# Performance work log

Measured on AMD Instinct MI355X. Metric: run time of the kernel, lower is better.

## Reference

```python
import jax, jax.numpy as jnp
import numpy as np

B, IN, ED, PW, OUT, CL, NK = 2048, 4096, 8192, 2048, 256, 16, 32
MIX = 0.5

def _onehot_mask(key, n):
    # near-one-hot selector matrix [n, NK], as built by forward_update_masks
    idx = jax.random.choice(key, n, (NK,), replace=False)
    return jnp.zeros((n, NK), jnp.float32).at[idx, jnp.arange(NK)].set(1.0)

def setup_inputs():
    ks = jax.random.split(jax.random.key(0), 24)
    f = jnp.float32
    adj = (jax.random.uniform(ks[4], (IN, IN)) < 0.01).astype(f)
    adj = jnp.maximum(adj, adj.T).at[jnp.arange(IN), jnp.arange(IN)].set(1.0)
    return {
        'x_gene': jax.random.normal(ks[0], (B, IN), f),
        'x_invmea': jax.random.normal(ks[1], (B, IN), f),
        'x_curv': jax.random.normal(ks[2], (B, ED), f),
        'clinn': jax.random.normal(ks[3], (B, CL), f),
        'Adj': adj,
        'edge_mask': (jax.random.uniform(ks[5], (ED, IN)) < 0.005).astype(f),
        'pathway_mask': (jax.random.uniform(ks[6], (PW, ED)) < 0.02).astype(f),
        'top_gene_mask': _onehot_mask(ks[7], IN),
        'top_invmea_mask': _onehot_mask(ks[8], IN),
        'top_curv_mask': _onehot_mask(ks[9], ED),
        'top_path_mask': _onehot_mask(ks[10], PW),
        'W1': jnp.full((IN, IN), 0.05, f),
        'b1': 0.01 * jax.random.normal(ks[11], (IN,), f),
        'W2': jnp.full((ED, IN), 0.05, f),
        'b2': 0.01 * jax.random.normal(ks[12], (ED,), f),
        'W3': jnp.full((PW, ED), 0.05, f),
        'b3': 0.01 * jax.random.normal(ks[13], (PW,), f),
        'W4': 0.02 * jax.random.normal(ks[14], (OUT, PW), f),
        'b4': 0.01 * jax.random.normal(ks[15], (OUT,), f),
        'W5': 0.02 * jax.random.normal(ks[16], (OUT, OUT), f),
        'b5': 0.01 * jax.random.normal(ks[17], (OUT,), f),
        'W6': 0.05 * jax.random.normal(ks[18], (OUT, OUT + CL + 4 * NK), f),
        'W7': 0.05 * jax.random.normal(ks[19], (1, OUT), f),
        'mp11': MIX * jnp.ones(IN, f),
        'mp12': (1.0 - MIX) * jnp.ones(IN, f),
        'mp1': jnp.ones(IN, f),
        'mp21': MIX * jnp.ones(ED, f),
        'mp22': (1.0 - MIX) * jnp.ones(ED, f),
        'mp2': jnp.ones(ED, f),
        'mp3': jnp.ones(PW, f),
    }

def reference(x_gene, x_invmea, x_curv, clinn, Adj, edge_mask, pathway_mask,
              top_gene_mask, top_invmea_mask, top_curv_mask, top_path_mask,
              W1, b1, W2, b2, W3, b3, W4, b4, W5, b5, W6, W7,
              mp11, mp12, mp1, mp21, mp22, mp2, mp3):
    sg = jax.lax.stop_gradient
    sig = jax.nn.sigmoid
    kept_gene = sg(x_gene @ top_gene_mask)                     # [B,NK] gather-as-matmul
    x1 = sig(x_gene @ (W1 * Adj).T + b1)                       # masked linear [B,IN]
    x1 = x_invmea * (mp11 * mp1) + x1 * (mp12 * mp1)
    kept_invmea = sg(x1 @ top_invmea_mask)
    x1 = sig(x1 @ (W2 * edge_mask).T + b2)                     # [B,ED]
    x1 = x_curv * (mp21 * mp2) + x1 * (mp22 * mp2)
    kept_curv = sg(x1 @ top_curv_mask)
    x1 = sig(x1 @ (W3 * pathway_mask).T + b3)                  # [B,PW]
    x1 = x1 * mp3
    kept_path = sg(x1 @ top_path_mask)
    x1 = sig(x1 @ W4.T + b4)
    x1 = sig(x1 @ W5.T + b5)                                   # [B,OUT]
    x_cat = jnp.concatenate([x1, kept_gene, kept_invmea, kept_curv, kept_path, clinn], axis=1)
    lp = sig(x_cat @ W6.T)
    lp = lp - jnp.mean(lp, axis=1, keepdims=True)
    return lp @ W7.T                                           # [B,1]
```

## Files before the change

kernel.cpp:

```cpp
#include <hip/hip_runtime.h>

typedef unsigned short u16;
typedef __attribute__((ext_vector_type(4))) float f32x4;
typedef __attribute__((ext_vector_type(8))) short s16x8;

__device__ __forceinline__ u16 f2bf(float f) {
    union { float f; unsigned u; } c; c.f = f;
    return (u16)((c.u + 0x7fffu + ((c.u >> 16) & 1u)) >> 16);
}
__device__ __forceinline__ float bf2f(u16 u) {
    union { unsigned u; float f; } c; c.u = ((unsigned)u) << 16; return c.f;
}
__device__ __forceinline__ unsigned pk2(float a, float b) {
    return (unsigned)f2bf(a) | ((unsigned)f2bf(b) << 16);
}
__device__ __forceinline__ float sigm(float x) { return 1.0f / (1.0f + __expf(-x)); }

__device__ __forceinline__ void load16_g2l(const void* g, void* l) {
    __builtin_amdgcn_global_load_lds(
        (const __attribute__((address_space(1))) unsigned int*)(unsigned long long)g,
        (__attribute__((address_space(3))) unsigned int*)(unsigned int)(unsigned long long)l,
        16, 0, 0);
}

__global__ __launch_bounds__(256) void convF(const float* __restrict__ in,
                                             u16* __restrict__ out, unsigned n8) {
    unsigned i = blockIdx.x * 256u + threadIdx.x;
    if (i >= n8) return;
    float4 a = ((const float4*)in)[2 * i];
    float4 b = ((const float4*)in)[2 * i + 1];
    uint4 o;
    o.x = pk2(a.x, a.y); o.y = pk2(a.z, a.w);
    o.z = pk2(b.x, b.y); o.w = pk2(b.z, b.w);
    ((uint4*)out)[i] = o;
}

__global__ __launch_bounds__(256) void transpF(const float* __restrict__ in,
                                               u16* __restrict__ out, int Rr, int Cc) {
    __shared__ float t[64][65];
    const int r0 = blockIdx.y * 64, c0 = blockIdx.x * 64;
    const int tid = threadIdx.x;
#pragma unroll
    for (int i = 0; i < 16; i++) {
        int idx = tid + i * 256;
        int rr = idx >> 6, cc = idx & 63;
        t[rr][cc] = in[(size_t)(r0 + rr) * Cc + c0 + cc];
    }
    __syncthreads();
#pragma unroll
    for (int i = 0; i < 16; i++) {
        int idx = tid + i * 256;
        int cc = idx >> 6, rr = idx & 63;
        out[(size_t)(c0 + cc) * Rr + r0 + rr] = f2bf(t[rr][cc]);
    }
}

__global__ __launch_bounds__(256) void transpB(const u16* __restrict__ in,
                                               u16* __restrict__ out, int Rr, int Cc) {
    __shared__ u16 t[64][66];
    const int r0 = blockIdx.y * 64, c0 = blockIdx.x * 64;
    const int tid = threadIdx.x;
#pragma unroll
    for (int i = 0; i < 16; i++) {
        int idx = tid + i * 256;
        int rr = idx >> 6, cc = idx & 63;
        t[rr][cc] = in[(size_t)(r0 + rr) * Cc + c0 + cc];
    }
    __syncthreads();
#pragma unroll
    for (int i = 0; i < 16; i++) {
        int idx = tid + i * 256;
        int cc = idx >> 6, rr = idx & 63;
        out[(size_t)(c0 + cc) * Rr + r0 + rr] = t[rr][cc];
    }
}

__global__ __launch_bounds__(256) void ell_build(const float* __restrict__ M,
                                                 const float* __restrict__ W,
                                                 unsigned* __restrict__ ell,
                                                 int* __restrict__ cnt,
                                                 int C, int PAD, int R) {
    const int lane = threadIdx.x & 63;
    const int row = blockIdx.x * 4 + (threadIdx.x >> 6);
    if (row >= R) return;
    const float* mrow = M + (size_t)row * C;
    const float* wrow = W + (size_t)row * C;
    int n = 0;
    for (int c = lane * 4; c < C; c += 256) {
        float4 m = *(const float4*)(mrow + c);
        n += (m.x != 0.f) + (m.y != 0.f) + (m.z != 0.f) + (m.w != 0.f);
    }
    int pre = n;
#pragma unroll
    for (int off = 1; off < 64; off <<= 1) {
        int t = __shfl_up(pre, off, 64);
        if (lane >= off) pre += t;
    }
    int s = pre - n;
    unsigned* erow = ell + (size_t)row * PAD;
    for (int c = lane * 4; c < C; c += 256) {
        float4 m = *(const float4*)(mrow + c);
        if (m.x != 0.f) { if (s < PAD) erow[s] = ((unsigned)f2bf(wrow[c + 0]) << 16) | (unsigned)(c + 0); s++; }
        if (m.y != 0.f) { if (s < PAD) erow[s] = ((unsigned)f2bf(wrow[c + 1]) << 16) | (unsigned)(c + 1); s++; }
        if (m.z != 0.f) { if (s < PAD) erow[s] = ((unsigned)f2bf(wrow[c + 2]) << 16) | (unsigned)(c + 2); s++; }
        if (m.w != 0.f) { if (s < PAD) erow[s] = ((unsigned)f2bf(wrow[c + 3]) << 16) | (unsigned)(c + 3); s++; }
    }
    int tot = __shfl(pre, 63, 64);
    if (lane == 0) cnt[row] = tot > PAD ? PAD : tot;
}

template <int BPL>
__global__ __launch_bounds__(256) void spmm(const unsigned* __restrict__ ell,
                                            const int* __restrict__ cnt,
                                            const u16* __restrict__ xT,
                                            u16* __restrict__ outT,
                                            const float* __restrict__ bias,
                                            const float* __restrict__ c1a,
                                            const float* __restrict__ c1b,
                                            const float* __restrict__ c2a,
                                            const float* __restrict__ c2b,
                                            const u16* __restrict__ invT,
                                            int PAD) {
    const int lane = threadIdx.x & 63;
    const int wv = __builtin_amdgcn_readfirstlane((int)(threadIdx.x >> 6));
    const int j = blockIdx.y * 4 + wv;
    const int b0 = blockIdx.x * (64 * BPL) + lane * BPL;

    const unsigned* ep = ell + (size_t)j * PAD;
    int len = cnt[j];
    if (len > PAD) len = PAD;

    float acc[BPL];
#pragma unroll
    for (int i = 0; i < BPL; i++) acc[i] = 0.f;

    auto body = [&](unsigned e) {
        const int k = (int)(e & 0xFFFFu);
        union { float f; unsigned u; } w; w.u = (e >> 16) << 16;
        const u16* xp = xT + (size_t)k * 2048 + b0;
        if (BPL == 4) {
            uint2 xv = *(const uint2*)xp;
            union { float f; unsigned u; } f0, f1, f2, f3;
            f0.u = xv.x << 16; f1.u = xv.x & 0xFFFF0000u;
            f2.u = xv.y << 16; f3.u = xv.y & 0xFFFF0000u;
            acc[0] += w.f * f0.f; acc[1] += w.f * f1.f;
            acc[2] += w.f * f2.f; acc[3] += w.f * f3.f;
        } else {
            unsigned xv = *(const unsigned*)xp;
            union { float f; unsigned u; } f0, f1;
            f0.u = xv << 16; f1.u = xv & 0xFFFF0000u;
            acc[0] += w.f * f0.f; acc[1] += w.f * f1.f;
        }
    };
    int s = 0;
    for (; s + 4 <= len; s += 4) {
        unsigned e0 = ep[s], e1 = ep[s + 1], e2 = ep[s + 2], e3 = ep[s + 3];
        body(e0); body(e1); body(e2); body(e3);
    }
    for (; s < len; ++s) body(ep[s]);

    const float bi = bias[j];
    float c1 = 0.f;
    if (c1a) { c1 = c1a[j]; if (c1b) c1 *= c1b[j]; }
    float c2 = 1.f;
    if (c2a) { c2 = c2a[j]; if (c2b) c2 *= c2b[j]; }

    float v[BPL];
#pragma unroll
    for (int i = 0; i < BPL; i++) v[i] = sigm(acc[i] + bi) * c2;
    if (invT) {
        const u16* ip = invT + (size_t)j * 2048 + b0;
        if (BPL == 4) {
            uint2 iv = *(const uint2*)ip;
            union { float f; unsigned u; } g0, g1, g2, g3;
            g0.u = iv.x << 16; g1.u = iv.x & 0xFFFF0000u;
            g2.u = iv.y << 16; g3.u = iv.y & 0xFFFF0000u;
            v[0] += g0.f * c1; v[1] += g1.f * c1;
            v[2] += g2.f * c1; v[3] += g3.f * c1;
        } else {
            unsigned iv = *(const unsigned*)ip;
            union { float f; unsigned u; } g0, g1;
            g0.u = iv << 16; g1.u = iv & 0xFFFF0000u;
            v[0] += g0.f * c1; v[1] += g1.f * c1;
        }
    }
    u16* op = outT + (size_t)j * 2048 + b0;
    if (BPL == 4) {
        uint2 ov; ov.x = pk2(v[0], v[1]); ov.y = pk2(v[2], v[3]);
        *(uint2*)op = ov;
    } else {
        *(unsigned*)op = pk2(v[0], v[1]);
    }
}

__global__ void init_idx(int* __restrict__ idx) {
    if (threadIdx.x < 128) idx[threadIdx.x] = 0;
}

__global__ __launch_bounds__(256) void find_idx(const float* __restrict__ mask,
                                                int n, int* __restrict__ out) {
    int k = blockIdx.x;
    for (int i = threadIdx.x; i < n; i += 256)
        if (mask[(size_t)i * 32 + k] != 0.0f) out[k] = i;
}

__global__ __launch_bounds__(256) void gatherFT(const float* __restrict__ src, int ld,
                                                const int* __restrict__ idx,
                                                u16* __restrict__ dstT) {
    int i = blockIdx.x * 256 + threadIdx.x;
    int kk = i >> 11, b = i & 2047;
    dstT[i] = f2bf(src[(size_t)b * ld + idx[kk]]);
}
__global__ __launch_bounds__(256) void gatherT(const u16* __restrict__ xT,
                                               const int* __restrict__ idx,
                                               u16* __restrict__ dstT) {
    int i = blockIdx.x * 256 + threadIdx.x;
    int kk = i >> 11, b = i & 2047;
    dstT[i] = xT[(size_t)idx[kk] * 2048 + b];
}

__global__ __launch_bounds__(256) void build_xcat(float* __restrict__ xcat,
                                                  const u16* __restrict__ x5,
                                                  const u16* __restrict__ kgT,
                                                  const u16* __restrict__ kiT,
                                                  const u16* __restrict__ kcT,
                                                  const u16* __restrict__ kpT,
                                                  const float* __restrict__ clinn) {
    int i = blockIdx.x * 256 + threadIdx.x;
    if (i >= 2048 * 400) return;
    int b = i / 400, c = i - b * 400;
    float v;
    if (c < 256)      v = bf2f(x5[b * 256 + c]);
    else if (c < 288) v = bf2f(kgT[(c - 256) * 2048 + b]);
    else if (c < 320) v = bf2f(kiT[(c - 288) * 2048 + b]);
    else if (c < 352) v = bf2f(kcT[(c - 320) * 2048 + b]);
    else if (c < 384) v = bf2f(kpT[(c - 352) * 2048 + b]);
    else              v = clinn[b * 16 + (c - 384)];
    xcat[i] = v;
}

template <int WR, int WC, int MF, int NF, int KC, int WPE>
__global__ __launch_bounds__(WR * WC * 64, WPE)
void gemm_t(const u16* __restrict__ A, const u16* __restrict__ W,
            u16* __restrict__ Out, const float* __restrict__ bias, int N, int K) {
    constexpr int NTHR = WR * WC * 64;
    constexpr int BM = WR * MF * 16;
    constexpr int BN = WC * NF * 16;
    constexpr int BK = KC * 32;
    constexpr int CPR = KC * 4;
    constexpr int MSK = CPR - 1;
    constexpr int CA = BM * CPR / NTHR;
    constexpr int CB = BN * CPR / NTHR;
    constexpr int L  = CA + CB;

    __shared__ u16 At[2][BM * BK];
    __shared__ u16 Bt[2][BN * BK];

    const int tid = threadIdx.x;
    const int lane = tid & 63;
    const int wave = tid >> 6;
    const int wr = wave / WC, wc = wave % WC;
    const int tn = blockIdx.x, tm = blockIdx.y;
    const int r16 = lane & 15;
    const int q = lane >> 4;

    const u16* aSrc[CA]; int aDst[CA];
#pragma unroll
    for (int j = 0; j < CA; j++) {
        int c = tid + j * NTHR;
        int r = c / CPR, p = c - r * CPR;
        aSrc[j] = A + (size_t)(tm * BM + r) * K + (p ^ (r & MSK)) * 8;
        aDst[j] = c * 8;
    }
    const u16* bSrc[CB]; int bDst[CB];
#pragma unroll
    for (int j = 0; j < CB; j++) {
        int c = tid + j * NTHR;
        int r = c / CPR, p = c - r * CPR;
        bSrc[j] = W + (size_t)(tn * BN + r) * K + (p ^ (r & MSK)) * 8;
        bDst[j] = c * 8;
    }
    int aRd[MF][KC], bRd[NF][KC];
#pragma unroll
    for (int mi = 0; mi < MF; mi++)
#pragma unroll
        for (int kc = 0; kc < KC; kc++)
            aRd[mi][kc] = (wr * MF * 16 + mi * 16 + r16) * BK + (((kc * 4 + q) ^ (r16 & MSK)) << 3);
#pragma unroll
    for (int ni = 0; ni < NF; ni++)
#pragma unroll
        for (int kc = 0; kc < KC; kc++)
            bRd[ni][kc] = (wc * NF * 16 + ni * 16 + r16) * BK + (((kc * 4 + q) ^ (r16 & MSK)) << 3);

    const int nIter = K / BK;

#define ISSUE(slot, it_)                                              \
    do {                                                              \
        const int k0_ = (it_) * BK;                                   \
        _Pragma("unroll")                                             \
        for (int j = 0; j < CA; j++)                                  \
            load16_g2l(aSrc[j] + k0_, &At[slot][aDst[j]]);            \
        _Pragma("unroll")                                             \
        for (int j = 0; j < CB; j++)                                  \
            load16_g2l(bSrc[j] + k0_, &Bt[slot][bDst[j]]);            \
    } while (0)

    ISSUE(0, 0);
    if (nIter > 1) ISSUE(1, 1);

    f32x4 acc[MF][NF];
#pragma unroll
    for (int i = 0; i < MF; i++)
#pragma unroll
        for (int j = 0; j < NF; j++) acc[i][j] = (f32x4){0.f, 0.f, 0.f, 0.f};

    for (int it = 0; it < nIter; ++it) {
        const int s = it & 1;
        if (it + 1 < nIter) __builtin_amdgcn_s_waitcnt(0xF70 | L);
        else                __builtin_amdgcn_s_waitcnt(0xF70);
        __asm__ volatile("" ::: "memory");
        __builtin_amdgcn_s_barrier();
        __asm__ volatile("" ::: "memory");

        s16x8 af[KC][MF], bfr[KC][NF];
#pragma unroll
        for (int kc = 0; kc < KC; kc++) {
#pragma unroll
            for (int mi = 0; mi < MF; mi++) af[kc][mi] = *(const s16x8*)(&At[s][aRd[mi][kc]]);
#pragma unroll
            for (int ni = 0; ni < NF; ni++) bfr[kc][ni] = *(const s16x8*)(&Bt[s][bRd[ni][kc]]);
        }
        __asm__ volatile("" ::: "memory");
        __builtin_amdgcn_s_waitcnt(0xC07F);
        __builtin_amdgcn_s_barrier();
        __asm__ volatile("" ::: "memory");

        if (it + 2 < nIter) ISSUE(s, it + 2);

#pragma unroll
        for (int kc = 0; kc < KC; kc++)
#pragma unroll
            for (int mi = 0; mi < MF; mi++)
#pragma unroll
                for (int ni = 0; ni < NF; ni++)
                    acc[mi][ni] = __builtin_amdgcn_mfma_f32_16x16x32_bf16(af[kc][mi], bfr[kc][ni], acc[mi][ni], 0, 0, 0);
    }
#undef ISSUE

#pragma unroll
    for (int ni = 0; ni < NF; ni++) {
        const int n = tn * BN + wc * NF * 16 + ni * 16 + r16;
        const float bi = bias ? bias[n] : 0.f;
#pragma unroll
        for (int mi = 0; mi < MF; mi++) {
#pragma unroll
            for (int rg = 0; rg < 4; rg++) {
                const int m = tm * BM + wr * MF * 16 + mi * 16 + q * 4 + rg;
                Out[(size_t)m * N + n] = f2bf(sigm(acc[mi][ni][rg] + bi));
            }
        }
    }
}

__global__ __launch_bounds__(256) void tail_k(const float* __restrict__ xcat,
                                              const float* __restrict__ W6,
                                              const float* __restrict__ W7,
                                              float* __restrict__ out) {
    __shared__ float xs[8 * 400];
    __shared__ float s1[4][8], s2[4][8], s3[4];
    const int tid = threadIdx.x;
    const int b0 = blockIdx.x * 8;
    for (int i = tid; i < 8 * 400; i += 256) {
        int r = i / 400, k = i - r * 400;
        xs[i] = xcat[(size_t)(b0 + r) * 400 + k];
    }
    __syncthreads();
    const int j = tid;
    float acc[8];
#pragma unroll
    for (int r = 0; r < 8; r++) acc[r] = 0.f;
    const float4* wrow = (const float4*)(W6 + (size_t)j * 400);
    for (int c = 0; c < 100; c++) {
        float4 wv = wrow[c];
        const float* wp = (const float*)&wv;
#pragma unroll
        for (int t = 0; t < 4; t++) {
            float w = wp[t];
            int k = c * 4 + t;
#pragma unroll
            for (int r = 0; r < 8; r++) acc[r] += w * xs[r * 400 + k];
        }
    }
    const float w7j = W7[j];
    const int lane = tid & 63, wave = tid >> 6;
    float t3 = w7j;
#pragma unroll
    for (int off = 32; off > 0; off >>= 1) t3 += __shfl_down(t3, off, 64);
    if (lane == 0) s3[wave] = t3;
#pragma unroll
    for (int r = 0; r < 8; r++) {
        float lp = sigm(acc[r]);
        float t1 = lp, t2 = lp * w7j;
#pragma unroll
        for (int off = 32; off > 0; off >>= 1) {
            t1 += __shfl_down(t1, off, 64);
            t2 += __shfl_down(t2, off, 64);
        }
        if (lane == 0) { s1[wave][r] = t1; s2[wave][r] = t2; }
    }
    __syncthreads();
    if (tid < 8) {
        float S1 = s1[0][tid] + s1[1][tid] + s1[2][tid] + s1[3][tid];
        float S2 = s2[0][tid] + s2[1][tid] + s2[2][tid] + s2[3][tid];
        float SW = s3[0] + s3[1] + s3[2] + s3[3];
        out[b0 + tid] = S2 - (S1 * (1.f / 256.f)) * SW;
    }
}

extern "C" void kernel_launch(void* const* d_in, const int* in_sizes, int n_in,
                              void* d_out, int out_size, void* d_ws, size_t ws_size,
                              hipStream_t stream) {
    const float* x_gene   = (const float*)d_in[0];
    const float* x_invmea = (const float*)d_in[1];
    const float* x_curv   = (const float*)d_in[2];
    const float* clinn    = (const float*)d_in[3];
    const float* Adj      = (const float*)d_in[4];
    const float* edge_m   = (const float*)d_in[5];
    const float* path_m   = (const float*)d_in[6];
    const float* tg_mask  = (const float*)d_in[7];
    const float* ti_mask  = (const float*)d_in[8];
    const float* tc_mask  = (const float*)d_in[9];
    const float* tp_mask  = (const float*)d_in[10];
    const float* W1 = (const float*)d_in[11];  const float* b1 = (const float*)d_in[12];
    const float* W2 = (const float*)d_in[13];  const float* b2 = (const float*)d_in[14];
    const float* W3 = (const float*)d_in[15];  const float* b3 = (const float*)d_in[16];
    const float* W4 = (const float*)d_in[17];  const float* b4 = (const float*)d_in[18];
    const float* W5 = (const float*)d_in[19];  const float* b5 = (const float*)d_in[20];
    const float* W6 = (const float*)d_in[21];
    const float* W7 = (const float*)d_in[22];
    const float* mp11 = (const float*)d_in[23];
    const float* mp12 = (const float*)d_in[24];
    const float* mp1  = (const float*)d_in[25];
    const float* mp21 = (const float*)d_in[26];
    const float* mp22 = (const float*)d_in[27];
    const float* mp2  = (const float*)d_in[28];
    const float* mp3  = (const float*)d_in[29];

    char* ws = (char*)d_ws;
    const float* nulf = nullptr;
    float* out = (float*)d_out;

    u16*  xTg   = (u16*)(ws + 0);
    float* xcat = (float*)(ws + 0);
    u16*  xinvT = (u16*)(ws + 16777216);
    u16*  xcvT  = (u16*)(ws + 33554432);
    u16*  x1T   = (u16*)(ws + 67108864);
    u16*  x2T   = (u16*)(ws + 83886080);
    u16*  x3T   = (u16*)(ws + 117440512);
    u16*  x3    = (u16*)(ws + 125829120);
    unsigned* ell1 = (unsigned*)(ws + 134217728);
    unsigned* ell2 = (unsigned*)(ws + 138412032);
    unsigned* ell3 = (unsigned*)(ws + 141557760);
    int* cnt1 = (int*)(ws + 144179200);
    int* cnt2 = (int*)(ws + 144195584);
    int* cnt3 = (int*)(ws + 144228352);
    int* idxg = (int*)(ws + 144236544);
    int* idxi = idxg + 32;
    int* idxc = idxg + 64;
    int* idxp = idxg + 96;
    u16* kgT  = (u16*)(ws + 144237056);
    u16* kiT  = (u16*)(ws + 144368128);
    u16* kcT  = (u16*)(ws + 144499200);
    u16* kpT  = (u16*)(ws + 144630272);
    u16* w4b  = (u16*)(ws + 144761344);
    u16* w5b  = (u16*)(ws + 145809920);
    u16* x4   = (u16*)(ws + 145940992);
    u16* x5   = (u16*)(ws + 146989568);

    init_idx<<<1, 128, 0, stream>>>(idxg);
    find_idx<<<32, 256, 0, stream>>>(tg_mask, 4096, idxg);
    find_idx<<<32, 256, 0, stream>>>(ti_mask, 4096, idxi);
    find_idx<<<32, 256, 0, stream>>>(tc_mask, 8192, idxc);
    find_idx<<<32, 256, 0, stream>>>(tp_mask, 2048, idxp);
    gatherFT<<<256, 256, 0, stream>>>(x_gene, 4096, idxg, kgT);

    transpF<<<dim3(64, 32), 256, 0, stream>>>(x_gene, xTg, 2048, 4096);
    transpF<<<dim3(64, 32), 256, 0, stream>>>(x_invmea, xinvT, 2048, 4096);
    transpF<<<dim3(128, 32), 256, 0, stream>>>(x_curv, xcvT, 2048, 8192);

    ell_build<<<1024, 256, 0, stream>>>(Adj,    W1, ell1, cnt1, 4096, 256, 4096);
    ell_build<<<2048, 256, 0, stream>>>(edge_m, W2, ell2, cnt2, 4096,  96, 8192);
    ell_build<<<512,  256, 0, stream>>>(path_m, W3, ell3, cnt3, 8192, 320, 2048);

    convF<<<256, 256, 0, stream>>>(W4, w4b, 65536u);
    convF<<<32, 256, 0, stream>>>(W5, w5b, 8192u);

    spmm<4><<<dim3(8, 1024), 256, 0, stream>>>(ell1, cnt1, xTg, x1T, b1,
                                               mp11, mp1, mp12, mp1, xinvT, 256);
    gatherT<<<256, 256, 0, stream>>>(x1T, idxi, kiT);

    spmm<4><<<dim3(8, 2048), 256, 0, stream>>>(ell2, cnt2, x1T, x2T, b2,
                                               mp21, mp2, mp22, mp2, xcvT, 96);
    gatherT<<<256, 256, 0, stream>>>(x2T, idxc, kcT);

    spmm<2><<<dim3(16, 512), 256, 0, stream>>>(ell3, cnt3, x2T, x3T, b3,
                                               nulf, nulf, mp3, nulf, (const u16*)nullptr, 320);
    gatherT<<<256, 256, 0, stream>>>(x3T, idxp, kpT);
    transpB<<<dim3(32, 32), 256, 0, stream>>>(x3T, x3, 2048, 2048);

    gemm_t<2, 4, 4, 2, 2, 4><<<dim3(2, 16), 512, 0, stream>>>(x3, w4b, x4, b4, 256, 2048);
    gemm_t<2, 4, 4, 2, 2, 4><<<dim3(2, 16), 512, 0, stream>>>(x4, w5b, x5, b5, 256, 256);

    build_xcat<<<3200, 256, 0, stream>>>(xcat, x5, kgT, kiT, kcT, kpT, clinn);
    tail_k<<<256, 256, 0, stream>>>(xcat, W6, W7, out);
}
```

Measured before the change: 1.016 ms.

## Merge index-finding kernels, use nontemporal spmm I/O, shrink gemm tiles

Replaces the init plus four find_idx launches with a single find_all kernel that does a block-wide max reduction. The spmm epilogue now uses nontemporal loads and stores for the streamed activation data. The W4/W5 GEMMs switch to smaller tiles with 256-thread blocks and four times as many blocks, to spread the small GEMMs over more compute units. These three changes each aim to cut launch overhead or improve cache use and occupancy, and the smaller tiles give up some data reuse in exchange.

```diff
diff --git a/kernel.cpp b/kernel.cpp
--- a/kernel.cpp
+++ b/kernel.cpp
@@ -171,14 +171,15 @@
     if (invT) {
         const u16* ip = invT + (size_t)j * 2048 + b0;
         if (BPL == 4) {
-            uint2 iv = *(const uint2*)ip;
+            unsigned long long iv = __builtin_nontemporal_load((const unsigned long long*)ip);
+            unsigned lo = (unsigned)iv, hi = (unsigned)(iv >> 32);
             union { float f; unsigned u; } g0, g1, g2, g3;
-            g0.u = iv.x << 16; g1.u = iv.x & 0xFFFF0000u;
-            g2.u = iv.y << 16; g3.u = iv.y & 0xFFFF0000u;
+            g0.u = lo << 16; g1.u = lo & 0xFFFF0000u;
+            g2.u = hi << 16; g3.u = hi & 0xFFFF0000u;
             v[0] += g0.f * c1; v[1] += g1.f * c1;
             v[2] += g2.f * c1; v[3] += g3.f * c1;
         } else {
-            unsigned iv = *(const unsigned*)ip;
+            unsigned iv = __builtin_nontemporal_load((const unsigned*)ip);
             union { float f; unsigned u; } g0, g1;
             g0.u = iv << 16; g1.u = iv & 0xFFFF0000u;
             v[0] += g0.f * c1; v[1] += g1.f * c1;
@@ -186,22 +187,40 @@
     }
     u16* op = outT + (size_t)j * 2048 + b0;
     if (BPL == 4) {
-        uint2 ov; ov.x = pk2(v[0], v[1]); ov.y = pk2(v[2], v[3]);
-        *(uint2*)op = ov;
+        unsigned long long ov = (unsigned long long)pk2(v[0], v[1])
+                              | ((unsigned long long)pk2(v[2], v[3]) << 32);
+        __builtin_nontemporal_store(ov, (unsigned long long*)op);
     } else {
-        *(unsigned*)op = pk2(v[0], v[1]);
-    }
-}
-
-__global__ void init_idx(int* __restrict__ idx) {
-    if (threadIdx.x < 128) idx[threadIdx.x] = 0;
-}
-
-__global__ __launch_bounds__(256) void find_idx(const float* __restrict__ mask,
-                                                int n, int* __restrict__ out) {
-    int k = blockIdx.x;
+        __builtin_nontemporal_store(pk2(v[0], v[1]), (unsigned*)op);
+    }
+}
+
+__global__ __launch_bounds__(256) void find_all(const float* __restrict__ m0, int n0,
+                                                const float* __restrict__ m1, int n1,
+                                                const float* __restrict__ m2, int n2,
+                                                const float* __restrict__ m3, int n3,
+                                                int* __restrict__ out) {
+    __shared__ int red[256];
+    const int g = blockIdx.x;
+    const int which = g >> 5, k = g & 31;
+    const float* mask; int n;
+    if (which == 0)      { mask = m0; n = n0; }
+    else if (which == 1) { mask = m1; n = n1; }
+    else if (which == 2) { mask = m2; n = n2; }
+    else                 { mask = m3; n = n3; }
+    int best = -1;
     for (int i = threadIdx.x; i < n; i += 256)
-        if (mask[(size_t)i * 32 + k] != 0.0f) out[k] = i;
+        if (mask[(size_t)i * 32 + k] != 0.0f) best = i;
+    red[threadIdx.x] = best;
+    __syncthreads();
+    for (int off = 128; off > 0; off >>= 1) {
+        if (threadIdx.x < off) {
+            int o = red[threadIdx.x + off];
+            if (o > red[threadIdx.x]) red[threadIdx.x] = o;
+        }
+        __syncthreads();
+    }
+    if (threadIdx.x == 0) out[which * 32 + k] = red[0] < 0 ? 0 : red[0];
 }
 
 __global__ __launch_bounds__(256) void gatherFT(const float* __restrict__ src, int ld,
@@ -477,11 +496,8 @@
     u16* x4   = (u16*)(ws + 145940992);
     u16* x5   = (u16*)(ws + 146989568);
 
-    init_idx<<<1, 128, 0, stream>>>(idxg);
-    find_idx<<<32, 256, 0, stream>>>(tg_mask, 4096, idxg);
-    find_idx<<<32, 256, 0, stream>>>(ti_mask, 4096, idxi);
-    find_idx<<<32, 256, 0, stream>>>(tc_mask, 8192, idxc);
-    find_idx<<<32, 256, 0, stream>>>(tp_mask, 2048, idxp);
+    find_all<<<128, 256, 0, stream>>>(tg_mask, 4096, ti_mask, 4096,
+                                      tc_mask, 8192, tp_mask, 2048, idxg);
     gatherFT<<<256, 256, 0, stream>>>(x_gene, 4096, idxg, kgT);
 
     transpF<<<dim3(64, 32), 256, 0, stream>>>(x_gene, xTg, 2048, 4096);
@@ -508,8 +524,8 @@
     gatherT<<<256, 256, 0, stream>>>(x3T, idxp, kpT);
     transpB<<<dim3(32, 32), 256, 0, stream>>>(x3T, x3, 2048, 2048);
 
-    gemm_t<2, 4, 4, 2, 2, 4><<<dim3(2, 16), 512, 0, stream>>>(x3, w4b, x4, b4, 256, 2048);
-    gemm_t<2, 4, 4, 2, 2, 4><<<dim3(2, 16), 512, 0, stream>>>(x4, w5b, x5, b5, 256, 256);
+    gemm_t<2, 2, 2, 2, 2, 4><<<dim3(4, 32), 256, 0, stream>>>(x3, w4b, x4, b4, 256, 2048);
+    gemm_t<2, 2, 2, 2, 2, 4><<<dim3(4, 32), 256, 0, stream>>>(x4, w5b, x5, b5, 256, 256);
 
     build_xcat<<<3200, 256, 0, stream>>>(xcat, x5, kgT, kiT, kcT, kpT, clinn);
     tail_k<<<256, 256, 0, stream>>>(xcat, W6, W7, out);
```

After: 992.9 us. 1.02x faster.
